# Kernel optimization log

Hardware: AMD Instinct MI355X
Metric: run time of the kernel (lower is better)

The kernel has to match this reference:

```python
import jax, jax.numpy as jnp
import numpy as np

EPS = 1e-07

def setup_inputs() -> dict:
    key = jax.random.key(0)
    k1, k2 = jax.random.split(key)
    B, C = 65536, 1000
    output = jax.random.normal(k1, (B, C), dtype=jnp.float32)
    target = jax.random.randint(k2, (B,), 0, C, dtype=jnp.int64)
    return {"output": output, "target": target}

def reference(output, target):
    B, C = output.shape
    # L2-normalize each row (p=2 norm over class dim) then softmax over classes
    norms = jnp.linalg.norm(output, axis=-1, keepdims=True) + EPS
    probs = jax.nn.softmax(output / norms, axis=1)  # [B, C]
    # per-class mean confidence [C]
    avg_conf = jnp.mean(probs, axis=0)
    # per-class empirical frequency [C] via one-hot-free bincount
    counts = jnp.zeros((C,), dtype=probs.dtype).at[target].add(1.0)
    avg_count = counts / B
    # mean absolute calibration gap over classes (scalar)
    return jnp.mean(jnp.abs(avg_conf - avg_count))
```

## Files before the change

### kernel.cpp

```cpp
#include <hip/hip_runtime.h>
#include <math.h>

#define TPB 512
#define NBLK 1024
#define CCLS 1000
#define NPART 32

__device__ __forceinline__ float wave_sum64(float x) {
  int t;
  t = __builtin_amdgcn_update_dpp(0, __float_as_int(x), 0x111, 0xf, 0xf, true); x += __int_as_float(t);
  t = __builtin_amdgcn_update_dpp(0, __float_as_int(x), 0x112, 0xf, 0xf, true); x += __int_as_float(t);
  t = __builtin_amdgcn_update_dpp(0, __float_as_int(x), 0x114, 0xf, 0xf, true); x += __int_as_float(t);
  t = __builtin_amdgcn_update_dpp(0, __float_as_int(x), 0x118, 0xf, 0xf, true); x += __int_as_float(t);
  t = __builtin_amdgcn_update_dpp(0, __float_as_int(x), 0x142, 0xa, 0xf, true); x += __int_as_float(t);
  t = __builtin_amdgcn_update_dpp(0, __float_as_int(x), 0x143, 0xc, 0xf, true); x += __int_as_float(t);
  return __int_as_float(__builtin_amdgcn_readlane(__float_as_int(x), 63));
}

__device__ __forceinline__ float coherent_load(const float* p) {
  return __hip_atomic_load(p, __ATOMIC_RELAXED, __HIP_MEMORY_SCOPE_AGENT);
}

__global__ __launch_bounds__(TPB, 8) void mdca_fused(const float* __restrict__ X,
                                                     const int* __restrict__ tgt,
                                                     float* __restrict__ g_ws,
                                                     float* __restrict__ out, int B) {
  __shared__ float sacc[1024];
  __shared__ float s_r[TPB / 64];
  __shared__ int s_last;
  const int t = threadIdx.x;
  const int lane = t & 63;
  const int wid = blockIdx.x * (TPB / 64) + (t >> 6);
  const int nw = NBLK * (TPB / 64);
  const bool v3 = (lane < 58);

  for (int i = t; i < 1024; i += TPB) sacc[i] = 0.f;

  float acc[16];
  #pragma unroll
  for (int i = 0; i < 16; ++i) acc[i] = 0.f;

  const float4 Z = make_float4(0.f, 0.f, 0.f, 0.f);

  for (int r = wid; r < B; r += nw) {
    const float4* b = reinterpret_cast<const float4*>(X + (size_t)r * CCLS);
    float4 a0 = b[lane];
    float4 a1 = b[64 + lane];
    float4 a2 = b[128 + lane];
    float4 a3 = v3 ? b[192 + lane] : Z;

    float ss = a0.x*a0.x + a0.y*a0.y + a0.z*a0.z + a0.w*a0.w
             + a1.x*a1.x + a1.y*a1.y + a1.z*a1.z + a1.w*a1.w
             + a2.x*a2.x + a2.y*a2.y + a2.z*a2.z + a2.w*a2.w
             + a3.x*a3.x + a3.y*a3.y + a3.z*a3.z + a3.w*a3.w;
    ss = wave_sum64(ss);

    const float inv = 1.0f / (sqrtf(ss) + 1e-7f);

    a0.x=__expf(a0.x*inv); a0.y=__expf(a0.y*inv); a0.z=__expf(a0.z*inv); a0.w=__expf(a0.w*inv);
    a1.x=__expf(a1.x*inv); a1.y=__expf(a1.y*inv); a1.z=__expf(a1.z*inv); a1.w=__expf(a1.w*inv);
    a2.x=__expf(a2.x*inv); a2.y=__expf(a2.y*inv); a2.z=__expf(a2.z*inv); a2.w=__expf(a2.w*inv);
    a3.x=__expf(a3.x*inv); a3.y=__expf(a3.y*inv); a3.z=__expf(a3.z*inv); a3.w=__expf(a3.w*inv);
    if (!v3) a3 = Z;

    float es = a0.x+a0.y+a0.z+a0.w + a1.x+a1.y+a1.z+a1.w
             + a2.x+a2.y+a2.z+a2.w + a3.x+a3.y+a3.z+a3.w;
    es = wave_sum64(es);

    const float invS = 1.0f / es;

    acc[0]  += a0.x*invS;  acc[1]  += a0.y*invS;  acc[2]  += a0.z*invS;  acc[3]  += a0.w*invS;
    acc[4]  += a1.x*invS;  acc[5]  += a1.y*invS;  acc[6]  += a1.z*invS;  acc[7]  += a1.w*invS;
    acc[8]  += a2.x*invS;  acc[9]  += a2.y*invS;  acc[10] += a2.z*invS;  acc[11] += a2.w*invS;
    acc[12] += a3.x*invS;  acc[13] += a3.y*invS;  acc[14] += a3.z*invS;  acc[15] += a3.w*invS;
  }

  __syncthreads();
  #pragma unroll
  for (int k = 0; k < 4; ++k)
    #pragma unroll
    for (int j = 0; j < 4; ++j)
      atomicAdd(&sacc[k * 256 + lane * 4 + j], acc[k * 4 + j]);

  if (t < 64) {
    for (int i = blockIdx.x * 64 + t; i < B; i += NBLK * 64)
      atomicAdd(&sacc[tgt[i]], -1.0f);
  }
  __syncthreads();

  float* part = g_ws + (size_t)(blockIdx.x & (NPART - 1)) * 1024;
  #pragma unroll
  for (int j = 0; j < 2; ++j) {
    int c = t * 2 + j;
    if (c < CCLS) atomicAdd(&part[c], sacc[c]);
  }

  __syncthreads();
  if (t == 0) {
    __threadfence();
    unsigned* dcnt = (unsigned*)(g_ws + NPART * 1024);
    unsigned old = __hip_atomic_fetch_add(dcnt, 1u, __ATOMIC_ACQ_REL,
                                          __HIP_MEMORY_SCOPE_AGENT);
    s_last = (old == (unsigned)(NBLK - 1));
  }
  __syncthreads();
  if (s_last) {
    const float invB = 1.0f / (float)B;
    float s = 0.f;
    for (int c = t; c < CCLS; c += TPB) {
      float v = 0.f;
      #pragma unroll
      for (int k = 0; k < NPART; ++k)
        v += coherent_load(&g_ws[k * 1024 + c]);
      s += fabsf(v * invB);
    }
    s = wave_sum64(s);
    if (lane == 0) s_r[t >> 6] = s;
    __syncthreads();
    if (t == 0) {
      float tot = 0.f;
      #pragma unroll
      for (int w = 0; w < TPB / 64; ++w) tot += s_r[w];
      out[0] = tot / (float)CCLS;
    }
  }
}

extern "C" void kernel_launch(void* const* d_in, const int* in_sizes, int n_in,
                              void* d_out, int out_size, void* d_ws, size_t ws_size,
                              hipStream_t stream) {
  const float* X = (const float*)d_in[0];
  const int* tgt = (const int*)d_in[1];
  const int B = in_sizes[1];

  float* g_ws = (float*)d_ws;

  hipMemsetAsync(d_ws, 0, (NPART * 1024 + 64) * sizeof(float), stream);
  mdca_fused<<<NBLK, TPB, 0, stream>>>(X, tgt, g_ws, (float*)d_out, B);
}
```

Before: 434.0 us.

## Replace atomic partials and last-block reduction with per-block stores and second kernel

Each block now writes its 1000-class partial vector to its own workspace slot with plain stores instead of atomically adding into 32 shared partial buffers. A separate reduce kernel sums the 1024 partials per class group and atomically adds the final abs-mean into the output. This removes global atomic contention, the done-counter fence, and the serial last-block tail. The cost is an extra kernel launch, a 4 MB partial buffer, and a memset on the output. The final sum is now built from float atomics in nondeterministic order.

After: 380.2 us. -12.4%, faster.

```diff
diff --git a/kernel.cpp b/kernel.cpp
--- a/kernel.cpp
+++ b/kernel.cpp
@@ -4,7 +4,6 @@
 #define TPB 512
 #define NBLK 1024
 #define CCLS 1000
-#define NPART 32
 
 __device__ __forceinline__ float wave_sum64(float x) {
   int t;
@@ -17,17 +16,10 @@
   return __int_as_float(__builtin_amdgcn_readlane(__float_as_int(x), 63));
 }
 
-__device__ __forceinline__ float coherent_load(const float* p) {
-  return __hip_atomic_load(p, __ATOMIC_RELAXED, __HIP_MEMORY_SCOPE_AGENT);
-}
-
-__global__ __launch_bounds__(TPB, 8) void mdca_fused(const float* __restrict__ X,
-                                                     const int* __restrict__ tgt,
-                                                     float* __restrict__ g_ws,
-                                                     float* __restrict__ out, int B) {
+__global__ __launch_bounds__(TPB, 8) void mdca_main(const float* __restrict__ X,
+                                                    const int* __restrict__ tgt,
+                                                    float* __restrict__ part, int B) {
   __shared__ float sacc[1024];
-  __shared__ float s_r[TPB / 64];
-  __shared__ int s_last;
   const int t = threadIdx.x;
   const int lane = t & 63;
   const int wid = blockIdx.x * (TPB / 64) + (t >> 6);
@@ -88,41 +80,42 @@
   }
   __syncthreads();
 
-  float* part = g_ws + (size_t)(blockIdx.x & (NPART - 1)) * 1024;
+  float* my = part + (size_t)blockIdx.x * 1024;
   #pragma unroll
   for (int j = 0; j < 2; ++j) {
     int c = t * 2 + j;
-    if (c < CCLS) atomicAdd(&part[c], sacc[c]);
+    if (c < CCLS) my[c] = sacc[c];
   }
+}
 
+__global__ __launch_bounds__(256) void mdca_reduce(const float* __restrict__ part,
+                                                   float* __restrict__ out, int B) {
+  __shared__ float4 sred[4];
+  const int t = threadIdx.x;
+  const float* p = part + 4 * blockIdx.x;
+
+  float4 s = make_float4(0.f, 0.f, 0.f, 0.f);
+  #pragma unroll
+  for (int j = 0; j < 4; ++j) {
+    const float4 v = *reinterpret_cast<const float4*>(p + (size_t)(t + 256 * j) * 1024);
+    s.x += v.x; s.y += v.y; s.z += v.z; s.w += v.w;
+  }
+  s.x = wave_sum64(s.x);
+  s.y = wave_sum64(s.y);
+  s.z = wave_sum64(s.z);
+  s.w = wave_sum64(s.w);
+  if ((t & 63) == 0) sred[t >> 6] = s;
   __syncthreads();
   if (t == 0) {
-    __threadfence();
-    unsigned* dcnt = (unsigned*)(g_ws + NPART * 1024);
-    unsigned old = __hip_atomic_fetch_add(dcnt, 1u, __ATOMIC_ACQ_REL,
-                                          __HIP_MEMORY_SCOPE_AGENT);
-    s_last = (old == (unsigned)(NBLK - 1));
-  }
-  __syncthreads();
-  if (s_last) {
+    float4 a = sred[0];
+    #pragma unroll
+    for (int w = 1; w < 4; ++w) {
+      a.x += sred[w].x; a.y += sred[w].y; a.z += sred[w].z; a.w += sred[w].w;
+    }
     const float invB = 1.0f / (float)B;
-    float s = 0.f;
-    for (int c = t; c < CCLS; c += TPB) {
-      float v = 0.f;
-      #pragma unroll
-      for (int k = 0; k < NPART; ++k)
-        v += coherent_load(&g_ws[k * 1024 + c]);
-      s += fabsf(v * invB);
-    }
-    s = wave_sum64(s);
-    if (lane == 0) s_r[t >> 6] = s;
-    __syncthreads();
-    if (t == 0) {
-      float tot = 0.f;
-      #pragma unroll
-      for (int w = 0; w < TPB / 64; ++w) tot += s_r[w];
-      out[0] = tot / (float)CCLS;
-    }
+    float r = fabsf(a.x * invB) + fabsf(a.y * invB)
+            + fabsf(a.z * invB) + fabsf(a.w * invB);
+    atomicAdd(out, r / (float)CCLS);
   }
 }
 
@@ -133,8 +126,9 @@
   const int* tgt = (const int*)d_in[1];
   const int B = in_sizes[1];
 
-  float* g_ws = (float*)d_ws;
+  float* part = (float*)d_ws;
 
-  hipMemsetAsync(d_ws, 0, (NPART * 1024 + 64) * sizeof(float), stream);
-  mdca_fused<<<NBLK, TPB, 0, stream>>>(X, tgt, g_ws, (float*)d_out, B);
+  hipMemsetAsync(d_out, 0, sizeof(float), stream);
+  mdca_main<<<NBLK, TPB, 0, stream>>>(X, tgt, part, B);
+  mdca_reduce<<<250, 256, 0, stream>>>(part, (float*)d_out, B);
 }
```
